# Performance work log

Hardware: AMD Instinct MI355X
Metric: run time of the kernel (lower is better)

## Reference

```python
import jax, jax.numpy as jnp
import numpy as np

EPS = 1e-6
R_DEPTH = 12   # CONFIG['max_recursion_depth']
STACK = 48     # CONFIG['stack_size']
GB, CG, CC = 0.8, 2.0, 0.25  # graph_bias_scale, context_gate_strength, commitment_cost


def _g(k, shape, s=0.05):
    return (jax.random.normal(k, shape) * s).astype(jnp.float32)


def setup_inputs():
    D, V, B, S = 128, 16384, 32, 128
    NS, NM = 64, 128
    ks = iter(jax.random.split(jax.random.key(0), 40))
    return {
        "input_ids": jax.random.randint(next(ks), (B, S), 0, V),
        "prev_syn_idx": jax.random.randint(next(ks), (B,), 0, NS),
        "prev_sem_idx": jax.random.randint(next(ks), (B,), 0, NM),
        "emb_mag": _g(next(ks), (V, D), 1.0),
        "emb_phase": _g(next(ks), (V, D), 1.0),
        "cell_Wr": _g(next(ks), (D, D)), "cell_Wi": _g(next(ks), (D, D)),
        "norm_scale": jnp.ones((D,), jnp.float32),
        "norm_shift": jnp.zeros((D,), jnp.float32),
        "modrelu_b": jnp.zeros((D,), jnp.float32),
        "qWr": _g(next(ks), (D, D)), "qWi": _g(next(ks), (D, D)),
        "kWr": _g(next(ks), (D, D)), "kWi": _g(next(ks), (D, D)),
        "vWr": _g(next(ks), (D, D)), "vWi": _g(next(ks), (D, D)),
        "oWr": _g(next(ks), (D, D)), "oWi": _g(next(ks), (D, D)),
        "halt_W": _g(next(ks), (2 * D, 1)),
        "halt_b": jnp.full((1,), -2.0, jnp.float32),  # nn.init.constant_(halt_linear.bias, -2.0)
        "stk_W": _g(next(ks), (2 * D, 3)), "stk_b": jnp.zeros((3,), jnp.float32),
        "cb_syn": _g(next(ks), (64, 2 * D), 1.0),
        "cb_sem": _g(next(ks), (128, 2 * D), 1.0),
        "ctxsyn_W": _g(next(ks), (2 * D, NS)), "ctxsyn_b": jnp.zeros((NS,), jnp.float32),
        "ctxsem_W": _g(next(ks), (2 * D, NM)), "ctxsem_b": jnp.zeros((NM,), jnp.float32),
        "adj_syn": _g(next(ks), (NS, NS), 1.0),
        "adj_sem": _g(next(ks), (NM, NM), 1.0),
        "gate_W": _g(next(ks), (4 * D, D)), "gate_b": jnp.zeros((D,), jnp.float32),
        "dec_W": _g(next(ks), (2 * D, V)), "dec_b": jnp.zeros((V,), jnp.float32),
    }


def _forward(fl, input_ids, prev_syn_idx, prev_sem_idx):
    (emb_mag, emb_phase, cell_Wr, cell_Wi, norm_scale, norm_shift, modrelu_b,
     qWr, qWi, kWr, kWi, vWr, vWi, oWr, oWi, halt_W, halt_b, stk_W, stk_b,
     cb_syn, cb_sem, ctxsyn_W, ctxsyn_b, ctxsem_W, ctxsem_b, adj_syn, adj_sem,
     gate_W, gate_b, dec_W, dec_b) = fl
    B = input_ids.shape[0]
    D = emb_mag.shape[1]
    sg = jax.lax.stop_gradient

    def clin(r, i, Wr, Wi):  # ComplexLinear (no bias)
        return r @ Wr - i @ Wi, i @ Wr + r @ Wi

    def cell(zr, zi):  # AdaptiveRecursiveCell
        r, i = clin(zr, zi, cell_Wr, cell_Wi)
        # ComplexLayerNorm (torch.var is unbiased -> ddof=1)
        mag = jnp.sqrt(r * r + i * i) + EPS
        mean = mag.mean(-1, keepdims=True)
        var = jnp.var(mag, axis=-1, ddof=1, keepdims=True)
        nm = (mag - mean) / jnp.sqrt(var + EPS) * norm_scale + norm_shift
        r, i = nm * r / mag, nm * i / mag  # cos/sin of original phase
        # ModReLU
        n = jnp.sqrt(r * r + i * i) + EPS
        s = jax.nn.relu(n + modrelu_b) / n
        r, i = r * s, i * s
        # MultiHeadComplexAttention: source computes Q,K but out = V -> o_proj(v_proj(z))
        vr, vi = clin(r, i, vWr, vWi)
        r, i = clin(vr, vi, oWr, oWi)
        zf = jnp.concatenate([r, i], -1)
        halt = jax.nn.sigmoid(zf @ halt_W + halt_b)          # [B,1]
        ctrl = jax.nn.softmax(zf @ stk_W + stk_b, axis=-1)   # [B,3]
        return r, i, halt, ctrl

    def stack_step(zr, zi, mem, ptr, ctrl):  # DifferentiableStack
        push, pop, noop = ctrl[:, 0:1], ctrl[:, 1:2], ctrl[:, 2:3]
        pu, pd = jnp.roll(ptr, 1, axis=1), jnp.roll(ptr, -1, axis=1)
        nptr = push * pu + pop * pd + noop * ptr
        nptr = nptr / (nptr.sum(1, keepdims=True) + EPS)
        zf = jnp.concatenate([zr, zi], -1)
        wm = (push * pu)[:, :, None]                          # write mask [B,STACK,1]
        mem = wm * zf[:, None, :] + mem * (1.0 - wm)
        read = (mem * nptr[:, :, None]).sum(1)                # [B,2D]
        return read[:, :D], read[:, D:], mem, nptr

    def gres(zr, zi, sr, si):  # GatedResidual, g_c = g + i*g
        g = jax.nn.sigmoid(jnp.concatenate([zr, zi, sr, si], -1) @ gate_W + gate_b)
        return ((1.0 - g) * zr + g * zi + g * (sr - si),
                (1.0 - g) * zi - g * zr + g * (si + sr))

    def vq(zr, zi, cb, adj, cW, cbias, pidx):  # ContextAwareDualVQ.vq_step (eval mode)
        zf = jnp.concatenate([zr, zi], -1)                    # [B,2D]
        d = (zf * zf).sum(1, keepdims=True) + (cb * cb).sum(1) - 2.0 * zf @ cb.T
        d = d - GB * jax.nn.sigmoid(adj[pidx]) - CG * jax.nn.softmax(zf @ cW + cbias, -1)
        idx = jnp.argmin(d, axis=1)
        zq = cb[idx]
        loss = jnp.mean((sg(zq) - zf) ** 2) + CC * jnp.mean((zq - sg(zf)) ** 2)
        return zf + sg(zq - zf), loss, idx                    # STE

    def step(carry, ids_t):
        mem, ptr, psyn, psem, lacc = carry
        r, th = emb_mag[ids_t], emb_phase[ids_t]              # embed
        zr, zi = r * jnp.cos(th), r * jnp.sin(th)
        rem = jnp.ones((B, 1), zr.dtype)
        accr = jnp.zeros_like(zr); acci = jnp.zeros_like(zi)
        slr = jnp.zeros_like(zr); sli = jnp.zeros_like(zi)
        for n in range(R_DEPTH):  # ACT recursion, halting-weighted accumulation
            pr, pi, halt, ctrl = cell(zr, zi)
            rr, ri, mem, ptr = stack_step(pr, pi, mem, ptr, ctrl)
            zr, zi = gres(pr, pi, rr, ri)
            w = rem if n == R_DEPTH - 1 else rem * halt
            accr, acci = accr + w * zr, acci + w * zi
            rem = rem * (1.0 - halt)
            slr, sli = slr + zr / R_DEPTH, sli + zi / R_DEPTH
        zqs, ls, isyn = vq(accr, acci, cb_syn, adj_syn, ctxsyn_W, ctxsyn_b, psyn)
        zqm, lm, isem = vq(slr, sli, cb_sem, adj_sem, ctxsem_W, ctxsem_b, psem)
        logits = 0.5 * (zqs + zqm) @ dec_W + dec_b            # decoder: Linear(2D, V)
        return (mem, ptr, isyn, isem, lacc + ls + lm), logits

    mem0 = jnp.zeros((B, STACK, 2 * D), jnp.float32)
    ptr0 = jnp.zeros((B, STACK), jnp.float32).at[:, 0].set(1.0)
    carry0 = (mem0, ptr0, prev_syn_idx, prev_sem_idx, jnp.zeros((), jnp.float32))
    (_, _, _, _, vq_loss), logits = jax.lax.scan(step, carry0, input_ids.T)
    return jnp.transpose(logits, (1, 0, 2)), vq_loss          # [B,S,V], scalar


def reference(input_ids, prev_syn_idx, prev_sem_idx, emb_mag, emb_phase, cell_Wr, cell_Wi, norm_scale, norm_shift, modrelu_b, qWr, qWi, kWr, kWi, vWr, vWi, oWr, oWi, halt_W, halt_b, stk_W, stk_b, cb_syn, cb_sem, ctxsyn_W, ctxsyn_b, ctxsem_W, ctxsem_b, adj_syn, adj_sem, gate_W, gate_b, dec_W, dec_b):
    fl = (emb_mag, emb_phase, cell_Wr, cell_Wi, norm_scale, norm_shift, modrelu_b,
          qWr, qWi, kWr, kWi, vWr, vWi, oWr, oWi, halt_W, halt_b, stk_W, stk_b,
          cb_syn, cb_sem, ctxsyn_W, ctxsyn_b, ctxsem_W, ctxsem_b, adj_syn, adj_sem,
          gate_W, gate_b, dec_W, dec_b)
    return _forward(fl, input_ids, prev_syn_idx, prev_sem_idx)
```

## Files before the change

kernel.cpp:

```cpp
#include <hip/hip_runtime.h>
#include <math.h>

#define D 128
#define D2 256
#define STK 48
#define SEQ 128
#define BATCH 32
#define RDPT 12
#define NSYN 64
#define NSEM 128
#define VOC 16384
#define EPSF 1e-6f
#define GB_C 0.8f
#define CG_C 2.0f

struct RParams {
  const int* input_ids;
  const int* prev_syn;
  const int* prev_sem;
  const float* emb_mag;
  const float* emb_phase;
  const float* cell_Wr;
  const float* cell_Wi;
  const float* norm_scale;
  const float* norm_shift;
  const float* modrelu_b;
  const float* VOr;
  const float* VOi;
  const float* halt_W;
  const float* halt_b;
  const float* stk_W;
  const float* stk_b;
  const float* cb_syn;
  const float* cb_sem;
  const float* ctxsyn_W;
  const float* ctxsyn_b;
  const float* ctxsem_W;
  const float* ctxsem_b;
  const float* gate_W;
  const float* gate_b;
  const float* cbT_syn;
  const float* cbT_sem;
  const float* cnrm_syn;
  const float* cnrm_sem;
  const float* gbsig_syn;
  const float* gbsig_sem;
  float* X;
  float* lossp;
};

__device__ __forceinline__ float waveAllSum(float v) {
  #pragma unroll
  for (int m = 32; m; m >>= 1) v += __shfl_xor(v, m);
  return v;
}

__global__ __launch_bounds__(512) void recur_kernel(RParams p) {
  __shared__ float4 VO4[(D / 2) * D];
  __shared__ float partr[512], parti[512];
  __shared__ alignas(16) float xr_[D], xi_[D], cr_[D], ci_[D];
  __shared__ float rAiA[D2], marr[D];
  __shared__ alignas(16) float zfc[D2], rd_[D2];
  __shared__ alignas(16) float acc2[D2], sl2[D2];
  __shared__ float zqs[D2];
  __shared__ float sptr[STK];
  __shared__ alignas(16) float nptrs[STK], wms[STK];
  __shared__ float hW_s[D2];
  __shared__ float stW_s[D2 * 3];
  __shared__ float scal[16];
  __shared__ int icb[2];
  __shared__ int ids[SEQ];

  const int tid = threadIdx.x;
  const int b = blockIdx.x;
  const int wv = tid >> 6;
  const int l = tid & 63;
  const int j = tid & 127;
  const int kq = tid >> 7;
  const int k0 = kq * 32;

  float cwr[32], cwi[32];
  #pragma unroll
  for (int kk = 0; kk < 32; ++kk) {
    cwr[kk] = p.cell_Wr[(size_t)(k0 + kk) * D + j];
    cwi[kk] = p.cell_Wi[(size_t)(k0 + kk) * D + j];
  }
  float gw[128];
  #pragma unroll
  for (int kk = 0; kk < 128; ++kk)
    gw[kk] = p.gate_W[(size_t)(kq * 128 + kk) * D + j];
  for (int e = tid; e < (D / 2) * D; e += 512) {
    const int kp = e >> 7;
    const int jj = e & 127;
    float4 w;
    w.x = p.VOr[(size_t)(2 * kp) * D + jj];
    w.y = p.VOi[(size_t)(2 * kp) * D + jj];
    w.z = p.VOr[(size_t)(2 * kp + 1) * D + jj];
    w.w = p.VOi[(size_t)(2 * kp + 1) * D + jj];
    VO4[e] = w;
  }
  float snsR = 0.f, nshR = 0.f, smbR = 0.f, sgbR = 0.f;
  if (tid < D) {
    snsR = p.norm_scale[tid];
    nshR = p.norm_shift[tid];
    smbR = p.modrelu_b[tid];
    sgbR = p.gate_b[tid];
  }
  if (tid < D2) hW_s[tid] = p.halt_W[tid];
  for (int e = tid; e < D2 * 3; e += 512) stW_s[e] = p.stk_W[e];
  if (tid < SEQ) ids[tid] = p.input_ids[(size_t)b * SEQ + tid];
  if (tid < STK) sptr[tid] = (tid == 0) ? 1.f : 0.f;
  if (tid == 0) { icb[0] = p.prev_syn[b]; icb[1] = p.prev_sem[b]; }
  const float hb = p.halt_b[0];
  const float sb0 = p.stk_b[0], sb1 = p.stk_b[1], sb2 = p.stk_b[2];

  float memv[24];
  #pragma unroll
  for (int q = 0; q < 24; ++q) memv[q] = 0.f;
  const int mdl = tid & 255, mjh = tid >> 8;
  float lossAcc = 0.f;
  float remv = 1.f;
  float mNxt = 0.f, pNxt = 0.f;
  __syncthreads();

  if (tid < D) {
    const int id0 = ids[0];
    mNxt = p.emb_mag[(size_t)id0 * D + tid];
    pNxt = p.emb_phase[(size_t)id0 * D + tid];
  }

  for (int t = 0; t < SEQ; ++t) {
    if (tid < D) {
      float sv, cv;
      sincosf(pNxt, &sv, &cv);
      xr_[tid] = mNxt * cv;
      xi_[tid] = mNxt * sv;
    }
    float accR = 0.f, accI = 0.f, slR = 0.f, slI = 0.f;
    if (tid < 64) remv = 1.f;
    __syncthreads();

    for (int n = 0; n < RDPT; ++n) {
      {
        const float4* x4r = (const float4*)(&xr_[k0]);
        const float4* x4i = (const float4*)(&xi_[k0]);
        float a0 = 0.f, a1 = 0.f, a2 = 0.f, a3 = 0.f;
        #pragma unroll
        for (int q = 0; q < 8; ++q) {
          float4 xa = x4r[q];
          float4 xb = x4i[q];
          a0 = fmaf(xa.x, cwr[q*4+0], a0); a0 = fmaf(-xb.x, cwi[q*4+0], a0);
          a1 = fmaf(xb.x, cwr[q*4+0], a1); a1 = fmaf(xa.x, cwi[q*4+0], a1);
          a2 = fmaf(xa.y, cwr[q*4+1], a2); a2 = fmaf(-xb.y, cwi[q*4+1], a2);
          a3 = fmaf(xb.y, cwr[q*4+1], a3); a3 = fmaf(xa.y, cwi[q*4+1], a3);
          a0 = fmaf(xa.z, cwr[q*4+2], a0); a0 = fmaf(-xb.z, cwi[q*4+2], a0);
          a1 = fmaf(xb.z, cwr[q*4+2], a1); a1 = fmaf(xa.z, cwi[q*4+2], a1);
          a2 = fmaf(xa.w, cwr[q*4+3], a2); a2 = fmaf(-xb.w, cwi[q*4+3], a2);
          a3 = fmaf(xb.w, cwr[q*4+3], a3); a3 = fmaf(xa.w, cwi[q*4+3], a3);
        }
        partr[tid] = a0 + a2;
        parti[tid] = a1 + a3;
      }
      __syncthreads();
      if (tid < D) {
        float rr = partr[tid] + partr[tid + 128] + partr[tid + 256] + partr[tid + 384];
        float ii = parti[tid] + parti[tid + 128] + parti[tid + 256] + parti[tid + 384];
        rAiA[tid] = rr;
        rAiA[tid + 128] = ii;
        marr[tid] = sqrtf(rr * rr + ii * ii) + EPSF;
      }
      __syncthreads();
      if (tid < 64) {
        float m0 = marr[l], m1 = marr[l + 64];
        float mean = waveAllSum(m0 + m1) * (1.f / D);
        float d0 = m0 - mean, d1 = m1 - mean;
        float v = waveAllSum(d0 * d0 + d1 * d1);
        if (l == 0) {
          scal[1] = mean;
          scal[2] = rsqrtf(v * (1.f / (D - 1)) + EPSF);
        }
      }
      __syncthreads();
      if (tid < D) {
        float m = marr[tid];
        float nm = (m - scal[1]) * scal[2] * snsR + nshR;
        float r_ = nm * rAiA[tid] / m;
        float i_ = nm * rAiA[tid + 128] / m;
        float nn = sqrtf(r_ * r_ + i_ * i_) + EPSF;
        float sc = fmaxf(nn + smbR, 0.f) / nn;
        cr_[tid] = r_ * sc;
        ci_[tid] = i_ * sc;
      }
      __syncthreads();
      {
        const float4* c4r = (const float4*)(&cr_[k0]);
        const float4* c4i = (const float4*)(&ci_[k0]);
        const float4* vbase = &VO4[(size_t)(k0 >> 1) * D + j];
        float a0 = 0.f, a1 = 0.f, a2 = 0.f, a3 = 0.f;
        #pragma unroll
        for (int q = 0; q < 8; ++q) {
          float4 xa = c4r[q];
          float4 xb = c4i[q];
          float4 wA = vbase[(size_t)(2 * q) * D];
          float4 wB = vbase[(size_t)(2 * q + 1) * D];
          a0 = fmaf(xa.x, wA.x, a0); a0 = fmaf(-xb.x, wA.y, a0);
          a1 = fmaf(xb.x, wA.x, a1); a1 = fmaf(xa.x, wA.y, a1);
          a2 = fmaf(xa.y, wA.z, a2); a2 = fmaf(-xb.y, wA.w, a2);
          a3 = fmaf(xb.y, wA.z, a3); a3 = fmaf(xa.y, wA.w, a3);
          a0 = fmaf(xa.z, wB.x, a0); a0 = fmaf(-xb.z, wB.y, a0);
          a1 = fmaf(xb.z, wB.x, a1); a1 = fmaf(xa.z, wB.y, a1);
          a2 = fmaf(xa.w, wB.z, a2); a2 = fmaf(-xb.w, wB.w, a2);
          a3 = fmaf(xb.w, wB.z, a3); a3 = fmaf(xa.w, wB.w, a3);
        }
        partr[tid] = a0 + a2;
        parti[tid] = a1 + a3;
      }
      __syncthreads();
      if (tid < 256) {
        if (tid < 128) {
          zfc[tid] = partr[tid] + partr[tid + 128] + partr[tid + 256] + partr[tid + 384];
        } else {
          const int d = tid - 128;
          zfc[tid] = parti[d] + parti[d + 128] + parti[d + 256] + parti[d + 384];
        }
      }
      __syncthreads();
      if (tid < 256) {
        float z0 = zfc[l], z1 = zfc[l + 64], z2 = zfc[l + 128], z3 = zfc[l + 192];
        float s;
        if (wv == 0) {
          s = z0 * hW_s[l] + z1 * hW_s[l + 64] + z2 * hW_s[l + 128] + z3 * hW_s[l + 192];
        } else {
          const int c = wv - 1;
          s = z0 * stW_s[l * 3 + c] + z1 * stW_s[(l + 64) * 3 + c] +
              z2 * stW_s[(l + 128) * 3 + c] + z3 * stW_s[(l + 192) * 3 + c];
        }
        s = waveAllSum(s);
        if (l == 0) scal[4 + wv] = s;
      }
      __syncthreads();
      if (tid < 64) {
        float halt = 1.f / (1.f + expf(-(scal[4] + hb)));
        float e0 = scal[5] + sb0, e1 = scal[6] + sb1, e2 = scal[7] + sb2;
        float mx = fmaxf(e0, fmaxf(e1, e2));
        float x0 = expf(e0 - mx), x1 = expf(e1 - mx), x2 = expf(e2 - mx);
        float sm = x0 + x1 + x2;
        float push = x0 / sm, pop = x1 / sm, noop = x2 / sm;
        float wgt = (n == RDPT - 1) ? remv : remv * halt;
        if (l == 0) scal[3] = wgt;
        remv = remv * (1.f - halt);
        float pj = 0.f, pu = 0.f, pd = 0.f;
        if (l < STK) {
          pj = sptr[l];
          pu = sptr[(l + STK - 1) % STK];
          pd = sptr[(l + 1) % STK];
        }
        float np_ = push * pu + pop * pd + noop * pj;
        float wm_ = push * pu;
        float ssum = waveAllSum((l < STK) ? np_ : 0.f);
        float inv = 1.f / (ssum + EPSF);
        if (l < STK) {
          np_ *= inv;
          nptrs[l] = np_;
          sptr[l] = np_;
          wms[l] = wm_;
        }
      }
      __syncthreads();
      {
        const float4* wm4 = (const float4*)wms;
        const float4* np4 = (const float4*)nptrs;
        float zfd = zfc[mdl];
        float accA = 0.f, accB = 0.f;
        #pragma unroll
        for (int m4 = 0; m4 < 6; ++m4) {
          float4 wmv = wm4[mjh * 6 + m4];
          float4 npv = np4[mjh * 6 + m4];
          const int base = m4 * 4;
          memv[base + 0] = wmv.x * zfd + memv[base + 0] * (1.f - wmv.x);
          accA = fmaf(memv[base + 0], npv.x, accA);
          memv[base + 1] = wmv.y * zfd + memv[base + 1] * (1.f - wmv.y);
          accB = fmaf(memv[base + 1], npv.y, accB);
          memv[base + 2] = wmv.z * zfd + memv[base + 2] * (1.f - wmv.z);
          accA = fmaf(memv[base + 2], npv.z, accA);
          memv[base + 3] = wmv.w * zfd + memv[base + 3] * (1.f - wmv.w);
          accB = fmaf(memv[base + 3], npv.w, accB);
        }
        partr[tid] = accA + accB;
      }
      __syncthreads();
      if (tid < D2) rd_[tid] = partr[tid] + partr[tid + 256];
      __syncthreads();
      {
        const float4* src4 = (kq < 2) ? (const float4*)(&zfc[kq * 128])
                                      : (const float4*)(&rd_[(kq - 2) * 128]);
        float g0 = 0.f, g1 = 0.f, g2 = 0.f, g3 = 0.f;
        #pragma unroll
        for (int q = 0; q < 32; ++q) {
          float4 xv = src4[q];
          g0 = fmaf(xv.x, gw[q * 4 + 0], g0);
          g1 = fmaf(xv.y, gw[q * 4 + 1], g1);
          g2 = fmaf(xv.z, gw[q * 4 + 2], g2);
          g3 = fmaf(xv.w, gw[q * 4 + 3], g3);
        }
        partr[tid] = (g0 + g1) + (g2 + g3);
      }
      __syncthreads();
      if (tid < D) {
        float g = partr[tid] + partr[tid + 128] + partr[tid + 256] +
                  partr[tid + 384] + sgbR;
        g = 1.f / (1.f + expf(-g));
        float pr_ = zfc[tid], pi_ = zfc[tid + 128];
        float rr_ = rd_[tid], ri_ = rd_[tid + 128];
        float nzr = (1.f - g) * pr_ + g * pi_ + g * (rr_ - ri_);
        float nzi = (1.f - g) * pi_ - g * pr_ + g * (ri_ + rr_);
        xr_[tid] = nzr;
        xi_[tid] = nzi;
        float wgt = scal[3];
        accR += wgt * nzr;
        accI += wgt * nzi;
        slR += nzr * (1.f / RDPT);
        slI += nzi * (1.f / RDPT);
      }
      __syncthreads();
    }

    if (tid < D) {
      const int idn = ids[(t + 1 < SEQ) ? t + 1 : t];
      mNxt = p.emb_mag[(size_t)idn * D + tid];
      pNxt = p.emb_phase[(size_t)idn * D + tid];
    }
    if (tid < D) {
      acc2[tid] = accR; acc2[tid + 128] = accI;
      sl2[tid] = slR;  sl2[tid + 128] = slI;
    }
    __syncthreads();

    {
      const int c = tid & 63, ch = tid >> 6;
      const int kb = ch * 32;
      const float* cb = p.cbT_syn + (size_t)kb * 64 + c;
      const float* cw = p.ctxsyn_W + (size_t)kb * 64 + c;
      const float4* a4 = (const float4*)(&acc2[kb]);
      float d0 = 0.f, d1 = 0.f, e0 = 0.f, e1 = 0.f;
      #pragma unroll
      for (int q = 0; q < 8; ++q) {
        float4 zv = a4[q];
        d0 = fmaf(cb[(size_t)(q * 4 + 0) * 64], zv.x, d0);
        e0 = fmaf(cw[(size_t)(q * 4 + 0) * 64], zv.x, e0);
        d1 = fmaf(cb[(size_t)(q * 4 + 1) * 64], zv.y, d1);
        e1 = fmaf(cw[(size_t)(q * 4 + 1) * 64], zv.y, e1);
        d0 = fmaf(cb[(size_t)(q * 4 + 2) * 64], zv.z, d0);
        e0 = fmaf(cw[(size_t)(q * 4 + 2) * 64], zv.z, e0);
        d1 = fmaf(cb[(size_t)(q * 4 + 3) * 64], zv.w, d1);
        e1 = fmaf(cw[(size_t)(q * 4 + 3) * 64], zv.w, e1);
      }
      partr[ch * 64 + c] = d0 + d1;
      parti[ch * 64 + c] = e0 + e1;
    }
    __syncthreads();
    if (tid < 64) {
      float dot = 0.f, e = p.ctxsyn_b[l];
      #pragma unroll
      for (int ch = 0; ch < 8; ++ch) {
        dot += partr[ch * 64 + l];
        e += parti[ch * 64 + l];
      }
      float d = p.cnrm_syn[l] - 2.f * dot;
      float m = e;
      #pragma unroll
      for (int mm = 32; mm; mm >>= 1) m = fmaxf(m, __shfl_xor(m, mm));
      float ex = expf(e - m);
      float s = waveAllSum(ex);
      const int pidx = icb[0];
      float score = d - p.gbsig_syn[(size_t)pidx * 64 + l] - CG_C * (ex / s);
      float bv = score; int bi = l;
      #pragma unroll
      for (int mm = 32; mm; mm >>= 1) {
        float ov = __shfl_xor(bv, mm); int oi = __shfl_xor(bi, mm);
        if (ov < bv || (ov == bv && oi < bi)) { bv = ov; bi = oi; }
      }
      if (l == 0) icb[0] = bi;
    }
    __syncthreads();
    if (tid < D2) {
      const int idx = icb[0];
      float zqv = p.cb_syn[(size_t)idx * D2 + tid];
      float df = zqv - acc2[tid];
      lossAcc += df * df;
      zqs[tid] = zqv;
    }
    {
      const int c = tid & 127, ch = tid >> 7;
      const int kb = ch * 64;
      const float* cb = p.cbT_sem + (size_t)kb * 128 + c;
      const float* cw = p.ctxsem_W + (size_t)kb * 128 + c;
      const float4* a4 = (const float4*)(&sl2[kb]);
      float d0 = 0.f, d1 = 0.f, e0 = 0.f, e1 = 0.f;
      #pragma unroll
      for (int q = 0; q < 16; ++q) {
        float4 zv = a4[q];
        d0 = fmaf(cb[(size_t)(q * 4 + 0) * 128], zv.x, d0);
        e0 = fmaf(cw[(size_t)(q * 4 + 0) * 128], zv.x, e0);
        d1 = fmaf(cb[(size_t)(q * 4 + 1) * 128], zv.y, d1);
        e1 = fmaf(cw[(size_t)(q * 4 + 1) * 128], zv.y, e1);
        d0 = fmaf(cb[(size_t)(q * 4 + 2) * 128], zv.z, d0);
        e0 = fmaf(cw[(size_t)(q * 4 + 2) * 128], zv.z, e0);
        d1 = fmaf(cb[(size_t)(q * 4 + 3) * 128], zv.w, d1);
        e1 = fmaf(cw[(size_t)(q * 4 + 3) * 128], zv.w, e1);
      }
      partr[ch * 128 + c] = d0 + d1;
      parti[ch * 128 + c] = e0 + e1;
    }
    __syncthreads();
    if (tid < 64) {
      float dot0 = 0.f, e0 = p.ctxsem_b[l];
      float dot1 = 0.f, e1 = p.ctxsem_b[l + 64];
      #pragma unroll
      for (int ch = 0; ch < 4; ++ch) {
        dot0 += partr[ch * 128 + l];       e0 += parti[ch * 128 + l];
        dot1 += partr[ch * 128 + l + 64];  e1 += parti[ch * 128 + l + 64];
      }
      float d0 = p.cnrm_sem[l] - 2.f * dot0;
      float d1 = p.cnrm_sem[l + 64] - 2.f * dot1;
      float m = fmaxf(e0, e1);
      #pragma unroll
      for (int mm = 32; mm; mm >>= 1) m = fmaxf(m, __shfl_xor(m, mm));
      float x0 = expf(e0 - m), x1 = expf(e1 - m);
      float s = waveAllSum(x0 + x1);
      const int pidx = icb[1];
      float s0 = d0 - p.gbsig_sem[(size_t)pidx * 128 + l] - CG_C * (x0 / s);
      float s1 = d1 - p.gbsig_sem[(size_t)pidx * 128 + l + 64] - CG_C * (x1 / s);
      float bv = s0; int bi = l;
      if (s1 < bv) { bv = s1; bi = l + 64; }
      #pragma unroll
      for (int mm = 32; mm; mm >>= 1) {
        float ov = __shfl_xor(bv, mm); int oi = __shfl_xor(bi, mm);
        if (ov < bv || (ov == bv && oi < bi)) { bv = ov; bi = oi; }
      }
      if (l == 0) icb[1] = bi;
    }
    __syncthreads();
    if (tid < D2) {
      const int idx = icb[1];
      float zqv = p.cb_sem[(size_t)idx * D2 + tid];
      float df = zqv - sl2[tid];
      lossAcc += df * df;
      p.X[(size_t)(b * SEQ + t) * D2 + tid] = 0.5f * (zqs[tid] + zqv);
    }
    __syncthreads();
  }

  partr[tid] = lossAcc;
  __syncthreads();
  if (tid < 256) partr[tid] += partr[tid + 256];
  __syncthreads();
  if (tid < 128) partr[tid] += partr[tid + 128];
  __syncthreads();
  if (tid < 64) {
    float v = partr[tid] + partr[tid + 64];
    v = waveAllSum(v);
    if (tid == 0) p.lossp[b] = v;
  }
}

__global__ __launch_bounds__(256) void voprod_kernel(const float* __restrict__ vr,
                                                     const float* __restrict__ vi,
                                                     const float* __restrict__ orr,
                                                     const float* __restrict__ oii,
                                                     float* __restrict__ VOr,
                                                     float* __restrict__ VOi) {
  __shared__ float a_r[D], a_i[D];
  const int k = blockIdx.x;
  const int tid = threadIdx.x;
  if (tid < D) { a_r[tid] = vr[k * D + tid]; a_i[tid] = vi[k * D + tid]; }
  __syncthreads();
  const int m = tid & 127;
  const int half = tid >> 7;
  float acc = 0.f;
  if (half == 0) {
    #pragma unroll 8
    for (int jj = 0; jj < D; ++jj)
      acc += a_r[jj] * orr[jj * D + m] - a_i[jj] * oii[jj * D + m];
    VOr[k * D + m] = acc;
  } else {
    #pragma unroll 8
    for (int jj = 0; jj < D; ++jj)
      acc += a_r[jj] * oii[jj * D + m] + a_i[jj] * orr[jj * D + m];
    VOi[k * D + m] = acc;
  }
}

__global__ void vqprep_kernel(const float* __restrict__ cb_syn,
                              const float* __restrict__ cb_sem,
                              const float* __restrict__ adj_syn,
                              const float* __restrict__ adj_sem,
                              float* __restrict__ cbT_syn,
                              float* __restrict__ cbT_sem,
                              float* __restrict__ cnrm_syn,
                              float* __restrict__ cnrm_sem,
                              float* __restrict__ gbsig_syn,
                              float* __restrict__ gbsig_sem) {
  const int tid = blockIdx.x * 256 + threadIdx.x;
  const int nt = gridDim.x * 256;
  for (int e = tid; e < NSYN * D2; e += nt) {
    int c = e / D2, k = e % D2;
    cbT_syn[k * NSYN + c] = cb_syn[e];
  }
  for (int e = tid; e < NSEM * D2; e += nt) {
    int c = e / D2, k = e % D2;
    cbT_sem[k * NSEM + c] = cb_sem[e];
  }
  for (int c = tid; c < NSYN; c += nt) {
    float s = 0.f;
    for (int k = 0; k < D2; ++k) { float v = cb_syn[c * D2 + k]; s += v * v; }
    cnrm_syn[c] = s;
  }
  for (int c = tid; c < NSEM; c += nt) {
    float s = 0.f;
    for (int k = 0; k < D2; ++k) { float v = cb_sem[c * D2 + k]; s += v * v; }
    cnrm_sem[c] = s;
  }
  for (int e = tid; e < NSYN * NSYN; e += nt)
    gbsig_syn[e] = GB_C / (1.f + expf(-adj_syn[e]));
  for (int e = tid; e < NSEM * NSEM; e += nt)
    gbsig_sem[e] = GB_C / (1.f + expf(-adj_sem[e]));
}

__global__ __launch_bounds__(256) void dec_kernel(const float* __restrict__ X,
                                                  const float* __restrict__ W,
                                                  const float* __restrict__ bias,
                                                  float* __restrict__ out) {
  __shared__ float A[32][D2];
  const int tid = threadIdx.x;
  const int bx = blockIdx.x;
  const int by = blockIdx.y;
  const float* xr = X + (size_t)by * 32 * D2;
  #pragma unroll
  for (int s = 0; s < 32; ++s) A[s][tid] = xr[s * D2 + tid];
  __syncthreads();
  const int ty = tid >> 5, tx = tid & 31;
  const int col0 = bx * 128 + tx * 4;
  const int r0 = ty * 4;
  float acc[4][4];
  #pragma unroll
  for (int r = 0; r < 4; ++r) {
    acc[r][0] = 0.f; acc[r][1] = 0.f; acc[r][2] = 0.f; acc[r][3] = 0.f;
  }
  const float* wp = W + col0;
  for (int k = 0; k < D2; k += 4) {
    float4 w0 = *(const float4*)(wp + (size_t)(k + 0) * VOC);
    float4 w1 = *(const float4*)(wp + (size_t)(k + 1) * VOC);
    float4 w2 = *(const float4*)(wp + (size_t)(k + 2) * VOC);
    float4 w3 = *(const float4*)(wp + (size_t)(k + 3) * VOC);
    #pragma unroll
    for (int r = 0; r < 4; ++r) {
      float4 a = *(const float4*)&A[r0 + r][k];
      acc[r][0] += a.x * w0.x + a.y * w1.x + a.z * w2.x + a.w * w3.x;
      acc[r][1] += a.x * w0.y + a.y * w1.y + a.z * w2.y + a.w * w3.y;
      acc[r][2] += a.x * w0.z + a.y * w1.z + a.z * w2.z + a.w * w3.z;
      acc[r][3] += a.x * w0.w + a.y * w1.w + a.z * w2.w + a.w * w3.w;
    }
  }
  float4 bv = *(const float4*)(bias + col0);
  #pragma unroll
  for (int r = 0; r < 4; ++r) {
    float4 o;
    o.x = acc[r][0] + bv.x; o.y = acc[r][1] + bv.y;
    o.z = acc[r][2] + bv.z; o.w = acc[r][3] + bv.w;
    *(float4*)(out + (size_t)(by * 32 + r0 + r) * VOC + col0) = o;
  }
}

__global__ void loss_kernel(const float* __restrict__ lp, float* __restrict__ out) {
  int l = threadIdx.x;
  float v = (l < BATCH) ? lp[l] : 0.f;
  #pragma unroll
  for (int off = 32; off; off >>= 1) v += __shfl_down(v, off);
  if (l == 0) out[0] = v * (1.25f / 8192.f);
}

extern "C" void kernel_launch(void* const* d_in, const int* in_sizes, int n_in,
                              void* d_out, int out_size, void* d_ws,
                              size_t ws_size, hipStream_t stream) {
  float* ws = (float*)d_ws;
  float* X = ws;
  float* lossp = X + 1048576;
  float* VOr = lossp + 64;
  float* VOi = VOr + 16384;
  float* cbT_syn = VOi + 16384;
  float* cbT_sem = cbT_syn + 16384;
  float* cnrm_syn = cbT_sem + 32768;
  float* cnrm_sem = cnrm_syn + 64;
  float* gbsig_syn = cnrm_sem + 128;
  float* gbsig_sem = gbsig_syn + 4096;

  RParams p;
  p.input_ids  = (const int*)d_in[0];
  p.prev_syn   = (const int*)d_in[1];
  p.prev_sem   = (const int*)d_in[2];
  p.emb_mag    = (const float*)d_in[3];
  p.emb_phase  = (const float*)d_in[4];
  p.cell_Wr    = (const float*)d_in[5];
  p.cell_Wi    = (const float*)d_in[6];
  p.norm_scale = (const float*)d_in[7];
  p.norm_shift = (const float*)d_in[8];
  p.modrelu_b  = (const float*)d_in[9];
  p.VOr        = VOr;
  p.VOi        = VOi;
  p.halt_W     = (const float*)d_in[18];
  p.halt_b     = (const float*)d_in[19];
  p.stk_W      = (const float*)d_in[20];
  p.stk_b      = (const float*)d_in[21];
  p.cb_syn     = (const float*)d_in[22];
  p.cb_sem     = (const float*)d_in[23];
  p.ctxsyn_W   = (const float*)d_in[24];
  p.ctxsyn_b   = (const float*)d_in[25];
  p.ctxsem_W   = (const float*)d_in[26];
  p.ctxsem_b   = (const float*)d_in[27];
  p.gate_W     = (const float*)d_in[30];
  p.gate_b     = (const float*)d_in[31];
  const float* dec_W = (const float*)d_in[32];
  const float* dec_b = (const float*)d_in[33];
  p.cbT_syn = cbT_syn;
  p.cbT_sem = cbT_sem;
  p.cnrm_syn = cnrm_syn;
  p.cnrm_sem = cnrm_sem;
  p.gbsig_syn = gbsig_syn;
  p.gbsig_sem = gbsig_sem;
  p.X = X;
  p.lossp = lossp;

  float* out = (float*)d_out;

  voprod_kernel<<<D, 256, 0, stream>>>((const float*)d_in[14], (const float*)d_in[15],
                                       (const float*)d_in[16], (const float*)d_in[17],
                                       VOr, VOi);
  vqprep_kernel<<<64, 256, 0, stream>>>((const float*)d_in[22], (const float*)d_in[23],
                                        (const float*)d_in[28], (const float*)d_in[29],
                                        cbT_syn, cbT_sem, cnrm_syn, cnrm_sem,
                                        gbsig_syn, gbsig_sem);
  recur_kernel<<<BATCH, 512, 0, stream>>>(p);
  dec_kernel<<<dim3(VOC / 128, BATCH * SEQ / 32), 256, 0, stream>>>(X, dec_W,
                                                                    dec_b, out);
  loss_kernel<<<1, 64, 0, stream>>>(lossp, out + (size_t)BATCH * SEQ * VOC);
}
```

Before: 18.20 ms.

## Swap VO and gate weight residency: VO in registers, fp16 gate in LDS

The fused VO weights (64 floats per thread) move from LDS into registers, and the gate weight matrix moves out of registers into LDS as fp16-packed uint4, prepacked by vqprep_kernel. This trades register pressure against LDS bandwidth for the gate matvec, and halves gate-weight LDS footprint through fp16 storage. The launch bound now requests 2 blocks per CU, which caps registers. Storing gate weights in fp16 adds rounding error to the gate pre-activation.

```diff
diff --git a/kernel.cpp b/kernel.cpp
--- a/kernel.cpp
+++ b/kernel.cpp
@@ -1,4 +1,5 @@
 #include <hip/hip_runtime.h>
+#include <hip/hip_fp16.h>
 #include <math.h>
 
 #define D 128
@@ -37,8 +38,8 @@
   const float* ctxsyn_b;
   const float* ctxsem_W;
   const float* ctxsem_b;
-  const float* gate_W;
   const float* gate_b;
+  const uint4* gatePk;
   const float* cbT_syn;
   const float* cbT_sem;
   const float* cnrm_syn;
@@ -55,8 +56,8 @@
   return v;
 }
 
-__global__ __launch_bounds__(512) void recur_kernel(RParams p) {
-  __shared__ float4 VO4[(D / 2) * D];
+__global__ __launch_bounds__(512, 2) void recur_kernel(RParams p) {
+  __shared__ uint4 gateLds[64 * D];
   __shared__ float partr[512], parti[512];
   __shared__ alignas(16) float xr_[D], xi_[D], cr_[D], ci_[D];
   __shared__ float rAiA[D2], marr[D];
@@ -79,26 +80,15 @@
   const int kq = tid >> 7;
   const int k0 = kq * 32;
 
-  float cwr[32], cwi[32];
+  float cwr[32], cwi[32], owr[32], owi[32];
   #pragma unroll
   for (int kk = 0; kk < 32; ++kk) {
     cwr[kk] = p.cell_Wr[(size_t)(k0 + kk) * D + j];
     cwi[kk] = p.cell_Wi[(size_t)(k0 + kk) * D + j];
-  }
-  float gw[128];
-  #pragma unroll
-  for (int kk = 0; kk < 128; ++kk)
-    gw[kk] = p.gate_W[(size_t)(kq * 128 + kk) * D + j];
-  for (int e = tid; e < (D / 2) * D; e += 512) {
-    const int kp = e >> 7;
-    const int jj = e & 127;
-    float4 w;
-    w.x = p.VOr[(size_t)(2 * kp) * D + jj];
-    w.y = p.VOi[(size_t)(2 * kp) * D + jj];
-    w.z = p.VOr[(size_t)(2 * kp + 1) * D + jj];
-    w.w = p.VOi[(size_t)(2 * kp + 1) * D + jj];
-    VO4[e] = w;
-  }
+    owr[kk] = p.VOr[(size_t)(k0 + kk) * D + j];
+    owi[kk] = p.VOi[(size_t)(k0 + kk) * D + j];
+  }
+  for (int e = tid; e < 64 * D; e += 512) gateLds[e] = p.gatePk[e];
   float snsR = 0.f, nshR = 0.f, smbR = 0.f, sgbR = 0.f;
   if (tid < D) {
     snsR = p.norm_scale[tid];
@@ -195,22 +185,19 @@
       {
         const float4* c4r = (const float4*)(&cr_[k0]);
         const float4* c4i = (const float4*)(&ci_[k0]);
-        const float4* vbase = &VO4[(size_t)(k0 >> 1) * D + j];
         float a0 = 0.f, a1 = 0.f, a2 = 0.f, a3 = 0.f;
         #pragma unroll
         for (int q = 0; q < 8; ++q) {
           float4 xa = c4r[q];
           float4 xb = c4i[q];
-          float4 wA = vbase[(size_t)(2 * q) * D];
-          float4 wB = vbase[(size_t)(2 * q + 1) * D];
-          a0 = fmaf(xa.x, wA.x, a0); a0 = fmaf(-xb.x, wA.y, a0);
-          a1 = fmaf(xb.x, wA.x, a1); a1 = fmaf(xa.x, wA.y, a1);
-          a2 = fmaf(xa.y, wA.z, a2); a2 = fmaf(-xb.y, wA.w, a2);
-          a3 = fmaf(xb.y, wA.z, a3); a3 = fmaf(xa.y, wA.w, a3);
-          a0 = fmaf(xa.z, wB.x, a0); a0 = fmaf(-xb.z, wB.y, a0);
-          a1 = fmaf(xb.z, wB.x, a1); a1 = fmaf(xa.z, wB.y, a1);
-          a2 = fmaf(xa.w, wB.z, a2); a2 = fmaf(-xb.w, wB.w, a2);
-          a3 = fmaf(xb.w, wB.z, a3); a3 = fmaf(xa.w, wB.w, a3);
+          a0 = fmaf(xa.x, owr[q*4+0], a0); a0 = fmaf(-xb.x, owi[q*4+0], a0);
+          a1 = fmaf(xb.x, owr[q*4+0], a1); a1 = fmaf(xa.x, owi[q*4+0], a1);
+          a2 = fmaf(xa.y, owr[q*4+1], a2); a2 = fmaf(-xb.y, owi[q*4+1], a2);
+          a3 = fmaf(xb.y, owr[q*4+1], a3); a3 = fmaf(xa.y, owi[q*4+1], a3);
+          a0 = fmaf(xa.z, owr[q*4+2], a0); a0 = fmaf(-xb.z, owi[q*4+2], a0);
+          a1 = fmaf(xb.z, owr[q*4+2], a1); a1 = fmaf(xa.z, owi[q*4+2], a1);
+          a2 = fmaf(xa.w, owr[q*4+3], a2); a2 = fmaf(-xb.w, owi[q*4+3], a2);
+          a3 = fmaf(xb.w, owr[q*4+3], a3); a3 = fmaf(xa.w, owi[q*4+3], a3);
         }
         partr[tid] = a0 + a2;
         parti[tid] = a1 + a3;
@@ -292,16 +279,25 @@
       if (tid < D2) rd_[tid] = partr[tid] + partr[tid + 256];
       __syncthreads();
       {
-        const float4* src4 = (kq < 2) ? (const float4*)(&zfc[kq * 128])
-                                      : (const float4*)(&rd_[(kq - 2) * 128]);
+        const float4* s4 = (kq < 2) ? (const float4*)(&zfc[kq * 128])
+                                    : (const float4*)(&rd_[(kq - 2) * 128]);
+        const uint4* g16 = &gateLds[(kq * 16) * D + j];
         float g0 = 0.f, g1 = 0.f, g2 = 0.f, g3 = 0.f;
         #pragma unroll
-        for (int q = 0; q < 32; ++q) {
-          float4 xv = src4[q];
-          g0 = fmaf(xv.x, gw[q * 4 + 0], g0);
-          g1 = fmaf(xv.y, gw[q * 4 + 1], g1);
-          g2 = fmaf(xv.z, gw[q * 4 + 2], g2);
-          g3 = fmaf(xv.w, gw[q * 4 + 3], g3);
+        for (int o = 0; o < 16; ++o) {
+          float4 xa = s4[2 * o];
+          float4 xb = s4[2 * o + 1];
+          uint4 w = g16[(size_t)o * D];
+          union { unsigned u; __half2 h; } c0, c1, c2, c3;
+          c0.u = w.x; c1.u = w.y; c2.u = w.z; c3.u = w.w;
+          float2 f0 = __half22float2(c0.h);
+          float2 f1 = __half22float2(c1.h);
+          float2 f2 = __half22float2(c2.h);
+          float2 f3 = __half22float2(c3.h);
+          g0 = fmaf(xa.x, f0.x, g0); g1 = fmaf(xa.y, f0.y, g1);
+          g2 = fmaf(xa.z, f1.x, g2); g3 = fmaf(xa.w, f1.y, g3);
+          g0 = fmaf(xb.x, f2.x, g0); g1 = fmaf(xb.y, f2.y, g1);
+          g2 = fmaf(xb.z, f3.x, g2); g3 = fmaf(xb.w, f3.y, g3);
         }
         partr[tid] = (g0 + g1) + (g2 + g3);
       }
@@ -495,12 +491,14 @@
                               const float* __restrict__ cb_sem,
                               const float* __restrict__ adj_syn,
                               const float* __restrict__ adj_sem,
+                              const float* __restrict__ gate_W,
                               float* __restrict__ cbT_syn,
                               float* __restrict__ cbT_sem,
                               float* __restrict__ cnrm_syn,
                               float* __restrict__ cnrm_sem,
                               float* __restrict__ gbsig_syn,
-                              float* __restrict__ gbsig_sem) {
+                              float* __restrict__ gbsig_sem,
+                              uint4* __restrict__ gatePk) {
   const int tid = blockIdx.x * 256 + threadIdx.x;
   const int nt = gridDim.x * 256;
   for (int e = tid; e < NSYN * D2; e += nt) {
@@ -525,6 +523,21 @@
     gbsig_syn[e] = GB_C / (1.f + expf(-adj_syn[e]));
   for (int e = tid; e < NSEM * NSEM; e += nt)
     gbsig_sem[e] = GB_C / (1.f + expf(-adj_sem[e]));
+  for (int e = tid; e < 64 * D; e += nt) {
+    int o = e / D, jj = e % D;
+    union { unsigned u; __half2 h; } w0, w1, w2, w3;
+    w0.h = __halves2half2(__float2half(gate_W[(size_t)(8 * o + 0) * D + jj]),
+                          __float2half(gate_W[(size_t)(8 * o + 1) * D + jj]));
+    w1.h = __halves2half2(__float2half(gate_W[(size_t)(8 * o + 2) * D + jj]),
+                          __float2half(gate_W[(size_t)(8 * o + 3) * D + jj]));
+    w2.h = __halves2half2(__float2half(gate_W[(size_t)(8 * o + 4) * D + jj]),
+                          __float2half(gate_W[(size_t)(8 * o + 5) * D + jj]));
+    w3.h = __halves2half2(__float2half(gate_W[(size_t)(8 * o + 6) * D + jj]),
+                          __float2half(gate_W[(size_t)(8 * o + 7) * D + jj]));
+    uint4 pk;
+    pk.x = w0.u; pk.y = w1.u; pk.z = w2.u; pk.w = w3.u;
+    gatePk[e] = pk;
+  }
 }
 
 __global__ __launch_bounds__(256) void dec_kernel(const float* __restrict__ X,
@@ -594,6 +607,7 @@
   float* cnrm_sem = cnrm_syn + 64;
   float* gbsig_syn = cnrm_sem + 128;
   float* gbsig_sem = gbsig_syn + 4096;
+  uint4* gatePk = (uint4*)(gbsig_sem + 16384);
 
   RParams p;
   p.input_ids  = (const int*)d_in[0];
@@ -618,8 +632,9 @@
   p.ctxsyn_b   = (const float*)d_in[25];
   p.ctxsem_W   = (const float*)d_in[26];
   p.ctxsem_b   = (const float*)d_in[27];
-  p.gate_W     = (const float*)d_in[30];
   p.gate_b     = (const float*)d_in[31];
+  p.gatePk     = gatePk;
+  const float* gate_W = (const float*)d_in[30];
   const float* dec_W = (const float*)d_in[32];
   const float* dec_b = (const float*)d_in[33];
   p.cbT_syn = cbT_syn;
@@ -638,8 +653,8 @@
                                        VOr, VOi);
   vqprep_kernel<<<64, 256, 0, stream>>>((const float*)d_in[22], (const float*)d_in[23],
                                         (const float*)d_in[28], (const float*)d_in[29],
-                                        cbT_syn, cbT_sem, cnrm_syn, cnrm_sem,
-                                        gbsig_syn, gbsig_sem);
+                                        gate_W, cbT_syn, cbT_sem, cnrm_syn,
+                                        cnrm_sem, gbsig_syn, gbsig_sem, gatePk);
   recur_kernel<<<BATCH, 512, 0, stream>>>(p);
   dec_kernel<<<dim3(VOC / 128, BATCH * SEQ / 32), 256, 0, stream>>>(X, dec_W,
                                                                     dec_b, out);
```

Result: faster. 15.46 ms (-15.0%).
